# Kernel optimization log

Hardware: AMD Instinct MI355X
Metric: run time of the kernel (lower is better)

## Reference

```python
import jax, jax.numpy as jnp
import numpy as np

Q_DIM = 1024
K_DIM = 1024
HID = 128
EPS = 1e-5


def setup_inputs() -> dict:
    key = jax.random.key(0)
    ks = jax.random.split(key, 12)
    B, Tq, Tk = 2, 512, 512
    s_q = 1.0 / np.sqrt(Q_DIM)
    s_k = 1.0 / np.sqrt(K_DIM)
    s_h3 = 1.0 / np.sqrt(3 * HID)
    s_h = 1.0 / np.sqrt(HID)
    return {
        "Q": jax.random.normal(ks[0], (B, Tq, Q_DIM), jnp.float32),
        "K": jax.random.normal(ks[1], (B, Tk, K_DIM), jnp.float32),
        "Wq": jax.random.uniform(ks[2], (Q_DIM, HID), jnp.float32, -s_q, s_q),
        "Wk": jax.random.uniform(ks[3], (K_DIM, HID), jnp.float32, -s_k, s_k),
        "ln_g": jnp.ones((3 * HID,), jnp.float32),
        "ln_b": jnp.zeros((3 * HID,), jnp.float32),
        "Wu": jax.random.uniform(ks[4], (3 * HID, HID), jnp.float32, -s_h3, s_h3),
        "bu": jax.random.uniform(ks[5], (HID,), jnp.float32, -s_h3, s_h3),
        "Wv": jax.random.uniform(ks[6], (3 * HID, HID), jnp.float32, -s_h3, s_h3),
        "bv": jax.random.uniform(ks[7], (HID,), jnp.float32, -s_h3, s_h3),
        "Wo": jax.random.uniform(ks[8], (HID, 1), jnp.float32, -s_h, s_h),
        "bo": jax.random.uniform(ks[9], (1,), jnp.float32, -s_h, s_h),
    }


def reference(Q, K, Wq, Wk, ln_g, ln_b, Wu, bu, Wv, bv, Wo, bo):
    B, Tq, _ = Q.shape
    Tk = K.shape[1]
    q = jnp.einsum("bqd,dh->bqh", Q, Wq)              # (B,Tq,H)
    k = jnp.einsum("bkd,dh->bkh", K, Wk)              # (B,Tk,H)
    q_exp = jnp.broadcast_to(q[:, :, None, :], (B, Tq, Tk, HID))
    k_exp = jnp.broadcast_to(k[:, None, :, :], (B, Tq, Tk, HID))
    x = jnp.concatenate([q_exp, k_exp, q_exp * k_exp], axis=-1)  # (B,Tq,Tk,3H)
    mu = jnp.mean(x, axis=-1, keepdims=True)
    var = jnp.mean(jnp.square(x - mu), axis=-1, keepdims=True)
    x = (x - mu) * jax.lax.rsqrt(var + EPS) * ln_g + ln_b
    u = jnp.einsum("bqkc,ch->bqkh", x, Wu) + bu
    v = jnp.einsum("bqkc,ch->bqkh", x, Wv) + bv
    z = u * jax.nn.gelu(v, approximate=False)
    return (jnp.einsum("bqkh,ho->bqko", z, Wo) + bo)[..., 0]  # (B,Tq,Tk)
```

## Files before the change

### kernel.cpp

```cpp
#include <hip/hip_runtime.h>
#include <hip/hip_bf16.h>
#include <math.h>


#define EPSLN 1e-5f

#define WS_QP   0
#define WS_KP   131072
#define WS_PU   262144
#define WS_PV   393216
#define WS_RU   524288
#define WS_RV   655360
#define WS_SQ   786432
#define WS_QQ   787456
#define WS_SK   788480
#define WS_KK   789504
#define WS_GUS  790528
#define WS_GVS  790656
#define WS_CU   790784
#define WS_CV   790912
#define WS_WTU  791040
#define WS_WTV  815616
#define WS_WQT  840192
#define WS_WKT  905728

typedef __attribute__((ext_vector_type(8))) short short8;
typedef __attribute__((ext_vector_type(4))) float f32x4;

__device__ inline unsigned short f2bf(float x) {
    unsigned u = __builtin_bit_cast(unsigned, x);
    unsigned r = u + 0x7fffu + ((u >> 16) & 1u);
    return (unsigned short)(r >> 16);
}
__device__ inline float b2f_lo(unsigned v) { return __builtin_bit_cast(float, v << 16); }
__device__ inline float b2f_hi(unsigned v) { return __builtin_bit_cast(float, v & 0xffff0000u); }
__device__ inline unsigned pack_bf2(float a, float b) {
    __hip_bfloat162 h = __float22bfloat162_rn(make_float2(a, b));
    unsigned r;
    __builtin_memcpy(&r, &h, 4);
    return r;
}
__device__ inline void store8(unsigned short* p, const unsigned short* v) {
    short8 s;
    #pragma unroll
    for (int e = 0; e < 8; ++e) s[e] = (short)v[e];
    *(short8*)p = s;
}
#define GELU_C1 2.3022035f
#define GELU_C2 0.1029431f
__device__ inline float fast_gelu(float v) {
    float ex = __builtin_amdgcn_exp2f(v * fmaf(v * v, GELU_C2, GELU_C1));
    float r  = __builtin_amdgcn_rcpf(ex + 1.f);
    return v - v * r;
}
#define BAR_LDS() asm volatile("s_waitcnt lgkmcnt(0)\n\ts_barrier" ::: "memory")

__global__ __launch_bounds__(256, 2)
void k_prep(const float* __restrict__ Wu, const float* __restrict__ bu,
            const float* __restrict__ Wv, const float* __restrict__ bv,
            const float* __restrict__ g, const float* __restrict__ bln,
            const float* __restrict__ Wo,
            const float* __restrict__ Wq, const float* __restrict__ Wk,
            float* __restrict__ ws) {
    int task = blockIdx.x, t = threadIdx.x;
    if (task < 2) {
        bool isV = task != 0;
        const float* W  = isV ? Wv : Wu;
        const float* bb = isV ? bv : bu;
        float* gout = ws + (isV ? WS_GVS : WS_GUS);
        float* cout = ws + (isV ? WS_CV : WS_CU);
        __shared__ float rg[2][128], rc[2][128];
        int tl = t & 127, g2 = t >> 7;
        float gu = 0.f, cu = 0.f;
        #pragma unroll 4
        for (int c = g2 * 192; c < g2 * 192 + 192; ++c) {
            float wv_ = W[c * 128 + tl];
            gu += g[c] * wv_;
            cu += bln[c] * wv_;
        }
        rg[g2][tl] = gu; rc[g2][tl] = cu;
        __syncthreads();
        if (t < 128) gout[t] = rg[0][t] + rg[1][t];
        else { int h = t - 128; cout[h] = rc[0][h] + rc[1][h] + bb[h]; }
    } else if (task < 8) {
        int tt = task - 2;
        bool isV = tt >= 3;
        int seg = tt % 3;
        const float* W = isV ? Wv : Wu;
        unsigned short* wt = (unsigned short*)(ws + (isV ? WS_WTV : WS_WTU));
        __shared__ unsigned short tile[128 * 130];
        for (int it = 0; it < 64; ++it) {
            int idx = t + 256 * it;
            int c = idx >> 7, h = idx & 127;
            float s = g[seg * 128 + c] * (isV ? 1.f : Wo[h]);
            tile[c * 130 + h] = f2bf(s * W[(seg * 128 + c) * 128 + h]);
        }
        __syncthreads();
        int h = t >> 1, c0 = (t & 1) * 64;
        for (int cc = 0; cc < 64; cc += 8) {
            unsigned short v[8];
            #pragma unroll
            for (int e = 0; e < 8; ++e) v[e] = tile[(c0 + cc + e) * 130 + h];
            store8(&wt[h * 384 + seg * 128 + c0 + cc], v);
        }
    } else {
        int tt = task - 8;
        const float* W = (tt >> 3) ? Wk : Wq;
        unsigned short* wt = (unsigned short*)(ws + ((tt >> 3) ? WS_WKT : WS_WQT));
        int seg = tt & 7;
        __shared__ unsigned short tile[128 * 130];
        for (int it = 0; it < 64; ++it) {
            int idx = t + 256 * it;
            int c = idx >> 7, h = idx & 127;
            tile[c * 130 + h] = f2bf(W[(size_t)(seg * 128 + c) * 128 + h]);
        }
        __syncthreads();
        int h = t >> 1, c0 = (t & 1) * 64;
        for (int cc = 0; cc < 64; cc += 8) {
            unsigned short v[8];
            #pragma unroll
            for (int e = 0; e < 8; ++e) v[e] = tile[(c0 + cc + e) * 130 + h];
            store8(&wt[h * 1024 + seg * 128 + c0 + cc], v);
        }
    }
}

#define XST 1028
#define QST 132
__global__ __launch_bounds__(256, 2)
void k_proj(const float* __restrict__ Q, const float* __restrict__ K,
            float* __restrict__ ws) {
    int blk = blockIdx.x, t = threadIdx.x;
    bool isK = blk >= 128;
    int r0 = (blk & 127) * 8;
    const float* src = isK ? K : Q;
    const unsigned short* wtin = (const unsigned short*)(ws + (isK ? WS_WKT : WS_WQT));
    float* dst = ws + (isK ? WS_KP : WS_QP);
    int L = t & 63, w = t >> 6;
    int col = L & 15, quad = L >> 4;

    __shared__ unsigned short XLb[16 * XST];
    __shared__ unsigned short qpL[16 * QST];
    __shared__ float sp1[16][4], sp2[16][4];

    {
        int srow = t >> 5;
        int c0 = (t & 31) * 4;
        const float* sp = src + (size_t)(r0 + srow) * 1024;
        #pragma unroll
        for (int g8 = 0; g8 < 8; ++g8) {
            float4 xv = *(const float4*)(sp + g8 * 128 + c0);
            unsigned* xp = (unsigned*)&XLb[srow * XST + g8 * 128 + c0];
            xp[0] = pack_bf2(xv.x, xv.y);
            xp[1] = pack_bf2(xv.z, xv.w);
        }
    }
    __syncthreads();

    f32x4 acc[2];
    acc[0] = (f32x4){0.f, 0.f, 0.f, 0.f};
    acc[1] = (f32x4){0.f, 0.f, 0.f, 0.f};
    #pragma unroll 4
    for (int ks = 0; ks < 32; ++ks) {
        short8 a = *(const short8*)&XLb[col * XST + ks * 32 + quad * 8];
        #pragma unroll
        for (int nt2 = 0; nt2 < 2; ++nt2) {
            int h = w * 32 + nt2 * 16 + col;
            short8 b = *(const short8*)&wtin[(size_t)h * 1024 + ks * 32 + quad * 8];
            acc[nt2] = __builtin_amdgcn_mfma_f32_16x16x32_bf16(a, b, acc[nt2], 0, 0, 0);
        }
    }

    #pragma unroll
    for (int r = 0; r < 4; ++r) {
        int row = quad * 4 + r;
        float s1 = acc[0][r] + acc[1][r];
        float s2 = acc[0][r] * acc[0][r] + acc[1][r] * acc[1][r];
        #pragma unroll
        for (int d = 1; d < 16; d <<= 1) { s1 += __shfl_xor(s1, d); s2 += __shfl_xor(s2, d); }
        if (col == 0) { sp1[row][w] = s1; sp2[row][w] = s2; }
        #pragma unroll
        for (int nt2 = 0; nt2 < 2; ++nt2) {
            int h = w * 32 + nt2 * 16 + col;
            qpL[row * QST + h] = f2bf(acc[nt2][r]);
            if (row < 8) dst[(size_t)(r0 + row) * 128 + h] = acc[nt2][r];
        }
    }
    __syncthreads();
    if (t < 8) {
        ws[(isK ? WS_SK : WS_SQ) + r0 + t] = (sp1[t][0] + sp1[t][1]) + (sp1[t][2] + sp1[t][3]);
        ws[(isK ? WS_KK : WS_QQ) + r0 + t] = (sp2[t][0] + sp2[t][1]) + (sp2[t][2] + sp2[t][3]);
    }

    int uv = w & 1, nhf = w >> 1;
    const unsigned short* wt = (const unsigned short*)(ws + (uv ? WS_WTV : WS_WTU));
    int cb0 = isK ? 128 : 0;
    f32x4 pacc[4];
    #pragma unroll
    for (int nt = 0; nt < 4; ++nt) pacc[nt] = (f32x4){0.f, 0.f, 0.f, 0.f};
    #pragma unroll
    for (int ks = 0; ks < 4; ++ks) {
        short8 a = *(const short8*)&qpL[col * QST + ks * 32 + quad * 8];
        #pragma unroll
        for (int nt = 0; nt < 4; ++nt) {
            int h = nhf * 64 + nt * 16 + col;
            short8 b = *(const short8*)&wt[h * 384 + cb0 + ks * 32 + quad * 8];
            pacc[nt] = __builtin_amdgcn_mfma_f32_16x16x32_bf16(a, b, pacc[nt], 0, 0, 0);
        }
    }
    float* PO = ws + (uv ? (isK ? WS_RV : WS_PV) : (isK ? WS_RU : WS_PU));
    #pragma unroll
    for (int nt = 0; nt < 4; ++nt)
        #pragma unroll
        for (int r = 0; r < 4; ++r) {
            int row = quad * 4 + r;
            if (row < 8)
                PO[(size_t)(r0 + row) * 128 + nhf * 64 + nt * 16 + col] = pacc[nt][r];
        }
}

#define ASTR 152
#define REDS 132
#define PST  136
__global__ __launch_bounds__(1024, 4)
void k_main(const float* __restrict__ ws, float* __restrict__ out,
            const float* __restrict__ Wo, const float* __restrict__ bo) {
    int blk = blockIdx.x;
    int jt = blk & 7, ig = (blk >> 3) & 31, b = blk >> 8;
    int t = threadIdx.x;
    int L = t & 63, w = t >> 6;
    int col = L & 15, quad = L >> 4;
    int jh = w >> 3, wh = w & 7;
    int krow0 = b * 512 + jt * 64;
    int jj = t >> 4, cb = (t & 15) * 8;
    int h = wh * 16 + col;

    __shared__ __align__(16) char smem[61440];
    unsigned short* Alds = (unsigned short*)smem;
    float*          red2 = (float*)(smem + 19456);
    unsigned short* QL   = (unsigned short*)smem;
    unsigned short* Q2L  = (unsigned short*)(smem + 4352);
    unsigned short* KL   = (unsigned short*)(smem + 8704);
    unsigned short* K2L  = (unsigned short*)(smem + 26112);
    float*          rsL2 = (float*)(smem + 53248);

    int bi0 = b * 512 + ig * 16;

    float kreg[8];
    {
        const float* kp = ws + WS_KP + (size_t)(krow0 + jj) * 128 + cb;
        #pragma unroll
        for (int e = 0; e < 8; ++e) kreg[e] = kp[e];
        unsigned kk4[4], k2[4];
        #pragma unroll
        for (int e = 0; e < 4; ++e) {
            kk4[e] = pack_bf2(kreg[e * 2], kreg[e * 2 + 1]);
            k2[e]  = pack_bf2(kreg[e * 2] * kreg[e * 2], kreg[e * 2 + 1] * kreg[e * 2 + 1]);
        }
        *(uint4*)&KL[jj * PST + cb]  = *(uint4*)&kk4[0];
        *(uint4*)&K2L[jj * PST + cb] = *(uint4*)&k2[0];
    }
    if (t < 512) {
        int row = t >> 5, c0 = (t & 31) * 4;
        float4 qv = *(const float4*)(ws + WS_QP + (size_t)(bi0 + row) * 128 + c0);
        unsigned q01 = pack_bf2(qv.x, qv.y), q23 = pack_bf2(qv.z, qv.w);
        unsigned s01 = pack_bf2(qv.x * qv.x, qv.y * qv.y);
        unsigned s23 = pack_bf2(qv.z * qv.z, qv.w * qv.w);
        uint2 qp = make_uint2(q01, q23), sp = make_uint2(s01, s23);
        *(uint2*)&QL[row * PST + c0]  = qp;
        *(uint2*)&Q2L[row * PST + c0] = sp;
    }
    unsigned prR[8];
    #pragma unroll
    for (int mt = 0; mt < 2; ++mt)
        #pragma unroll
        for (int r = 0; r < 4; ++r) {
            int jl = jh * 32 + mt * 16 + quad * 4 + r;
            float ru = ws[WS_RU + (size_t)(krow0 + jl) * 128 + h];
            float rv = ws[WS_RV + (size_t)(krow0 + jl) * 128 + h];
            prR[mt * 4 + r] = pack_bf2(ru, rv);
        }

    short8 w3f[2][4];
    {
        const unsigned short* wtu = (const unsigned short*)(ws + WS_WTU);
        const unsigned short* wtv = (const unsigned short*)(ws + WS_WTV);
        #pragma unroll
        for (int ks = 0; ks < 4; ++ks) {
            w3f[0][ks] = *(const short8*)&wtu[h * 384 + 256 + ks * 32 + quad * 8];
            w3f[1][ks] = *(const short8*)&wtv[h * 384 + 256 + ks * 32 + quad * 8];
        }
    }
    float wo  = Wo[h];
    float gusv = ws[WS_GUS + h] * wo;
    float cuv  = ws[WS_CU + h] * wo;
    float gvsv = ws[WS_GVS + h];
    float cvv  = ws[WS_CV + h];
    float bo0 = bo[0];

    const float* qpBase = ws + WS_QP + (size_t)bi0 * 128 + cb;
    const float* puBase = ws + WS_PU + (size_t)bi0 * 128 + h;
    const float* pvBase = ws + WS_PV + (size_t)bi0 * 128 + h;
    float4 qA = *(const float4*)(qpBase);
    float4 qB = *(const float4*)(qpBase + 4);
    float puv = puBase[0];
    float pvv = pvBase[0];
    __syncthreads();

    if (w < 4) {
        int j = w * 16 + col;
        f32x4 d1a = (f32x4){0.f, 0.f, 0.f, 0.f};
        f32x4 d2a = (f32x4){0.f, 0.f, 0.f, 0.f};
        #pragma unroll
        for (int ks = 0; ks < 4; ++ks) {
            short8 aq  = *(const short8*)&QL[col * PST + ks * 32 + quad * 8];
            short8 bk  = *(const short8*)&KL[j * PST + ks * 32 + quad * 8];
            d1a = __builtin_amdgcn_mfma_f32_16x16x32_bf16(aq, bk, d1a, 0, 0, 0);
            short8 aq2 = *(const short8*)&Q2L[col * PST + ks * 32 + quad * 8];
            short8 bk2 = *(const short8*)&K2L[j * PST + ks * 32 + quad * 8];
            d2a = __builtin_amdgcn_mfma_f32_16x16x32_bf16(aq2, bk2, d2a, 0, 0, 0);
        }
        float skj = ws[WS_SK + krow0 + j];
        float kkj = ws[WS_KK + krow0 + j];
        #pragma unroll
        for (int r = 0; r < 4; ++r) {
            int i = quad * 4 + r;
            float mu = (ws[WS_SQ + bi0 + i] + skj + d1a[r]) * (1.0f / 384.0f);
            float e2 = (ws[WS_QQ + bi0 + i] + kkj + d2a[r]) * (1.0f / 384.0f);
            float rs = rsqrtf(e2 - mu * mu + EPSLN);
            *(float2*)&rsL2[(i * 64 + j) * 2] = make_float2(rs, rs * mu);
        }
    }
    __syncthreads();

    #pragma unroll 2
    for (int ii = 0; ii < 16; ++ii) {
        float4 qA2 = *(const float4*)(qpBase + (ii + 1) * 128);
        float4 qB2 = *(const float4*)(qpBase + (ii + 1) * 128 + 4);
        float pu2 = puBase[(ii + 1) * 128];
        float pv2 = pvBase[(ii + 1) * 128];
        {
            unsigned pk[4];
            float x0 = kreg[0] * qA.x, x1 = kreg[1] * qA.y;
            float x2 = kreg[2] * qA.z, x3 = kreg[3] * qA.w;
            float y0 = kreg[4] * qB.x, y1 = kreg[5] * qB.y;
            float y2 = kreg[6] * qB.z, y3 = kreg[7] * qB.w;
            pk[0] = pack_bf2(x0, x1); pk[1] = pack_bf2(x2, x3);
            pk[2] = pack_bf2(y0, y1); pk[3] = pack_bf2(y2, y3);
            unsigned* arow = (unsigned*)Alds + jj * (ASTR / 2) + cb / 2;
            *(uint4*)&arow[0] = *(uint4*)&pk[0];
        }
        BAR_LDS();
        f32x4 acc[2][2];
        #pragma unroll
        for (int mt = 0; mt < 2; ++mt) {
            acc[mt][0] = (f32x4){puv, puv, puv, puv};
            acc[mt][1] = (f32x4){pvv, pvv, pvv, pvv};
        }
        #pragma unroll
        for (int ks = 0; ks < 4; ++ks) {
            short8 a0 = *(const short8*)&Alds[(jh * 32 + col) * ASTR + ks * 32 + quad * 8];
            short8 a1 = *(const short8*)&Alds[(jh * 32 + col + 16) * ASTR + ks * 32 + quad * 8];
            acc[0][0] = __builtin_amdgcn_mfma_f32_16x16x32_bf16(a0, w3f[0][ks], acc[0][0], 0, 0, 0);
            acc[0][1] = __builtin_amdgcn_mfma_f32_16x16x32_bf16(a0, w3f[1][ks], acc[0][1], 0, 0, 0);
            acc[1][0] = __builtin_amdgcn_mfma_f32_16x16x32_bf16(a1, w3f[0][ks], acc[1][0], 0, 0, 0);
            acc[1][1] = __builtin_amdgcn_mfma_f32_16x16x32_bf16(a1, w3f[1][ks], acc[1][1], 0, 0, 0);
        }
        #pragma unroll
        for (int mt = 0; mt < 2; ++mt) {
            int jb = jh * 32 + mt * 16 + quad * 4;
            float4 s0 = *(const float4*)&rsL2[(ii * 64 + jb) * 2];
            float4 s1 = *(const float4*)&rsL2[(ii * 64 + jb) * 2 + 4];
            #pragma unroll
            for (int r = 0; r < 4; ++r) {
                float rs   = r == 0 ? s0.x : r == 1 ? s0.z : r == 2 ? s1.x : s1.z;
                float rsmu = r == 0 ? s0.y : r == 1 ? s0.w : r == 2 ? s1.y : s1.w;
                int jl = jb + r;
                unsigned pr = prR[mt * 4 + r];
                float su  = acc[mt][0][r] + b2f_lo(pr);
                float u   = fmaf(rs, su, fmaf(-rsmu, gusv, cuv));
                float sv_ = acc[mt][1][r] + b2f_hi(pr);
                float v   = fmaf(rs, sv_, fmaf(-rsmu, gvsv, cvv));
                red2[jl * REDS + wh * 16 + col] = u * fast_gelu(v);
            }
        }
        BAR_LDS();
        if (t < 512) {
            const float4* rr = (const float4*)&red2[(t >> 3) * REDS];
            int k = t & 7;
            float s = 0.f;
            #pragma unroll
            for (int c4 = 0; c4 < 4; ++c4) {
                float4 x = rr[k + c4 * 8];
                s += (x.x + x.y) + (x.z + x.w);
            }
            s += __shfl_xor(s, 1);
            s += __shfl_xor(s, 2);
            s += __shfl_xor(s, 4);
            if (k == 0)
                out[(size_t)(bi0 + ii) * 512 + jt * 64 + (t >> 3)] = s + bo0;
        }
        qA = qA2; qB = qB2; puv = pu2; pvv = pv2;
    }
}

extern "C" void kernel_launch(void* const* d_in, const int* in_sizes, int n_in,
                              void* d_out, int out_size, void* d_ws, size_t ws_size,
                              hipStream_t stream) {
    const float* Q   = (const float*)d_in[0];
    const float* K   = (const float*)d_in[1];
    const float* Wq  = (const float*)d_in[2];
    const float* Wk  = (const float*)d_in[3];
    const float* g   = (const float*)d_in[4];
    const float* bln = (const float*)d_in[5];
    const float* Wu  = (const float*)d_in[6];
    const float* bu  = (const float*)d_in[7];
    const float* Wv  = (const float*)d_in[8];
    const float* bv  = (const float*)d_in[9];
    const float* Wo  = (const float*)d_in[10];
    const float* bo  = (const float*)d_in[11];
    float* ws  = (float*)d_ws;
    float* out = (float*)d_out;

    hipLaunchKernelGGL(k_prep, dim3(24), dim3(256), 0, stream, Wu, bu, Wv, bv, g, bln, Wo, Wq, Wk, ws);
    hipLaunchKernelGGL(k_proj, dim3(256), dim3(256), 0, stream, Q, K, ws);
    hipLaunchKernelGGL(k_main, dim3(512), dim3(1024), 0, stream, ws, out, Wo, bo);
}
```

Baseline: 187.4 us.

## Halve k_main block tile and double-buffer LDS to drop one barrier per row

Each k_main block now covers 32 key columns with 512 threads instead of 64 with 1024, and the grid doubles to 1024 blocks. The A tile and the reduction buffer are double-buffered, and the row reduction for step ii-1 is deferred into step ii. That removes the second LDS barrier per iteration and lets the reduction overlap the next MFMA stage, with a final epilogue reduction after the loop. The cost is more blocks that each repeat setup work (loading K, Q, weights and the rs table) and more LDS per block.

```diff
diff --git a/kernel.cpp b/kernel.cpp
--- a/kernel.cpp
+++ b/kernel.cpp
@@ -222,27 +222,28 @@
 #define ASTR 152
 #define REDS 132
 #define PST  136
-__global__ __launch_bounds__(1024, 4)
+__global__ __launch_bounds__(512, 4)
 void k_main(const float* __restrict__ ws, float* __restrict__ out,
             const float* __restrict__ Wo, const float* __restrict__ bo) {
     int blk = blockIdx.x;
-    int jt = blk & 7, ig = (blk >> 3) & 31, b = blk >> 8;
+    int jt = blk & 15, ig = (blk >> 4) & 31, b = blk >> 9;
     int t = threadIdx.x;
     int L = t & 63, w = t >> 6;
     int col = L & 15, quad = L >> 4;
-    int jh = w >> 3, wh = w & 7;
-    int krow0 = b * 512 + jt * 64;
+    int krow0 = b * 512 + jt * 32;
     int jj = t >> 4, cb = (t & 15) * 8;
-    int h = wh * 16 + col;
-
-    __shared__ __align__(16) char smem[61440];
-    unsigned short* Alds = (unsigned short*)smem;
-    float*          red2 = (float*)(smem + 19456);
-    unsigned short* QL   = (unsigned short*)smem;
-    unsigned short* Q2L  = (unsigned short*)(smem + 4352);
-    unsigned short* KL   = (unsigned short*)(smem + 8704);
-    unsigned short* K2L  = (unsigned short*)(smem + 26112);
-    float*          rsL2 = (float*)(smem + 53248);
+    int h = w * 16 + col;
+
+    __shared__ __align__(16) char smem[57344];
+    unsigned short* Alds0 = (unsigned short*)smem;
+    unsigned short* Alds1 = (unsigned short*)(smem + 9728);
+    float*          red20 = (float*)(smem + 19456);
+    float*          red21 = (float*)(smem + 36352);
+    unsigned short* QL    = (unsigned short*)smem;
+    unsigned short* Q2L   = (unsigned short*)(smem + 4352);
+    unsigned short* KL    = (unsigned short*)(smem + 8704);
+    unsigned short* K2L   = (unsigned short*)(smem + 17408);
+    float*          rsL2  = (float*)(smem + 53248);
 
     int bi0 = b * 512 + ig * 16;
 
@@ -260,7 +261,7 @@
         *(uint4*)&KL[jj * PST + cb]  = *(uint4*)&kk4[0];
         *(uint4*)&K2L[jj * PST + cb] = *(uint4*)&k2[0];
     }
-    if (t < 512) {
+    {
         int row = t >> 5, c0 = (t & 31) * 4;
         float4 qv = *(const float4*)(ws + WS_QP + (size_t)(bi0 + row) * 128 + c0);
         unsigned q01 = pack_bf2(qv.x, qv.y), q23 = pack_bf2(qv.z, qv.w);
@@ -275,7 +276,7 @@
     for (int mt = 0; mt < 2; ++mt)
         #pragma unroll
         for (int r = 0; r < 4; ++r) {
-            int jl = jh * 32 + mt * 16 + quad * 4 + r;
+            int jl = mt * 16 + quad * 4 + r;
             float ru = ws[WS_RU + (size_t)(krow0 + jl) * 128 + h];
             float rv = ws[WS_RV + (size_t)(krow0 + jl) * 128 + h];
             prR[mt * 4 + r] = pack_bf2(ru, rv);
@@ -307,7 +308,7 @@
     float pvv = pvBase[0];
     __syncthreads();
 
-    if (w < 4) {
+    if (w < 2) {
         int j = w * 16 + col;
         f32x4 d1a = (f32x4){0.f, 0.f, 0.f, 0.f};
         f32x4 d2a = (f32x4){0.f, 0.f, 0.f, 0.f};
@@ -328,13 +329,16 @@
             float mu = (ws[WS_SQ + bi0 + i] + skj + d1a[r]) * (1.0f / 384.0f);
             float e2 = (ws[WS_QQ + bi0 + i] + kkj + d2a[r]) * (1.0f / 384.0f);
             float rs = rsqrtf(e2 - mu * mu + EPSLN);
-            *(float2*)&rsL2[(i * 64 + j) * 2] = make_float2(rs, rs * mu);
+            *(float2*)&rsL2[(i * 32 + j) * 2] = make_float2(rs, rs * mu);
         }
     }
     __syncthreads();
 
     #pragma unroll 2
     for (int ii = 0; ii < 16; ++ii) {
+        unsigned short* Ap = (ii & 1) ? Alds1 : Alds0;
+        float* Rp = (ii & 1) ? red21 : red20;
+        float* Rq = (ii & 1) ? red20 : red21;
         float4 qA2 = *(const float4*)(qpBase + (ii + 1) * 128);
         float4 qB2 = *(const float4*)(qpBase + (ii + 1) * 128 + 4);
         float pu2 = puBase[(ii + 1) * 128];
@@ -347,7 +351,7 @@
             float y2 = kreg[6] * qB.z, y3 = kreg[7] * qB.w;
             pk[0] = pack_bf2(x0, x1); pk[1] = pack_bf2(x2, x3);
             pk[2] = pack_bf2(y0, y1); pk[3] = pack_bf2(y2, y3);
-            unsigned* arow = (unsigned*)Alds + jj * (ASTR / 2) + cb / 2;
+            unsigned* arow = (unsigned*)Ap + jj * (ASTR / 2) + cb / 2;
             *(uint4*)&arow[0] = *(uint4*)&pk[0];
         }
         BAR_LDS();
@@ -359,34 +363,15 @@
         }
         #pragma unroll
         for (int ks = 0; ks < 4; ++ks) {
-            short8 a0 = *(const short8*)&Alds[(jh * 32 + col) * ASTR + ks * 32 + quad * 8];
-            short8 a1 = *(const short8*)&Alds[(jh * 32 + col + 16) * ASTR + ks * 32 + quad * 8];
+            short8 a0 = *(const short8*)&Ap[col * ASTR + ks * 32 + quad * 8];
+            short8 a1 = *(const short8*)&Ap[(col + 16) * ASTR + ks * 32 + quad * 8];
             acc[0][0] = __builtin_amdgcn_mfma_f32_16x16x32_bf16(a0, w3f[0][ks], acc[0][0], 0, 0, 0);
             acc[0][1] = __builtin_amdgcn_mfma_f32_16x16x32_bf16(a0, w3f[1][ks], acc[0][1], 0, 0, 0);
             acc[1][0] = __builtin_amdgcn_mfma_f32_16x16x32_bf16(a1, w3f[0][ks], acc[1][0], 0, 0, 0);
             acc[1][1] = __builtin_amdgcn_mfma_f32_16x16x32_bf16(a1, w3f[1][ks], acc[1][1], 0, 0, 0);
         }
-        #pragma unroll
-        for (int mt = 0; mt < 2; ++mt) {
-            int jb = jh * 32 + mt * 16 + quad * 4;
-            float4 s0 = *(const float4*)&rsL2[(ii * 64 + jb) * 2];
-            float4 s1 = *(const float4*)&rsL2[(ii * 64 + jb) * 2 + 4];
-            #pragma unroll
-            for (int r = 0; r < 4; ++r) {
-                float rs   = r == 0 ? s0.x : r == 1 ? s0.z : r == 2 ? s1.x : s1.z;
-                float rsmu = r == 0 ? s0.y : r == 1 ? s0.w : r == 2 ? s1.y : s1.w;
-                int jl = jb + r;
-                unsigned pr = prR[mt * 4 + r];
-                float su  = acc[mt][0][r] + b2f_lo(pr);
-                float u   = fmaf(rs, su, fmaf(-rsmu, gusv, cuv));
-                float sv_ = acc[mt][1][r] + b2f_hi(pr);
-                float v   = fmaf(rs, sv_, fmaf(-rsmu, gvsv, cvv));
-                red2[jl * REDS + wh * 16 + col] = u * fast_gelu(v);
-            }
-        }
-        BAR_LDS();
-        if (t < 512) {
-            const float4* rr = (const float4*)&red2[(t >> 3) * REDS];
+        if (ii > 0 && t < 256) {
+            const float4* rr = (const float4*)&Rq[(t >> 3) * REDS];
             int k = t & 7;
             float s = 0.f;
             #pragma unroll
@@ -398,9 +383,43 @@
             s += __shfl_xor(s, 2);
             s += __shfl_xor(s, 4);
             if (k == 0)
-                out[(size_t)(bi0 + ii) * 512 + jt * 64 + (t >> 3)] = s + bo0;
+                out[(size_t)(bi0 + ii - 1) * 512 + jt * 32 + (t >> 3)] = s + bo0;
+        }
+        #pragma unroll
+        for (int mt = 0; mt < 2; ++mt) {
+            int jb = mt * 16 + quad * 4;
+            float4 s0 = *(const float4*)&rsL2[(ii * 32 + jb) * 2];
+            float4 s1 = *(const float4*)&rsL2[(ii * 32 + jb) * 2 + 4];
+            #pragma unroll
+            for (int r = 0; r < 4; ++r) {
+                float rs   = r == 0 ? s0.x : r == 1 ? s0.z : r == 2 ? s1.x : s1.z;
+                float rsmu = r == 0 ? s0.y : r == 1 ? s0.w : r == 2 ? s1.y : s1.w;
+                int jl = jb + r;
+                unsigned pr = prR[mt * 4 + r];
+                float su  = acc[mt][0][r] + b2f_lo(pr);
+                float u   = fmaf(rs, su, fmaf(-rsmu, gusv, cuv));
+                float sv_ = acc[mt][1][r] + b2f_hi(pr);
+                float v   = fmaf(rs, sv_, fmaf(-rsmu, gvsv, cvv));
+                Rp[jl * REDS + w * 16 + col] = u * fast_gelu(v);
+            }
         }
         qA = qA2; qB = qB2; puv = pu2; pvv = pv2;
+    }
+    BAR_LDS();
+    if (t < 256) {
+        const float4* rr = (const float4*)&red21[(t >> 3) * REDS];
+        int k = t & 7;
+        float s = 0.f;
+        #pragma unroll
+        for (int c4 = 0; c4 < 4; ++c4) {
+            float4 x = rr[k + c4 * 8];
+            s += (x.x + x.y) + (x.z + x.w);
+        }
+        s += __shfl_xor(s, 1);
+        s += __shfl_xor(s, 2);
+        s += __shfl_xor(s, 4);
+        if (k == 0)
+            out[(size_t)(bi0 + 15) * 512 + jt * 32 + (t >> 3)] = s + bo0;
     }
 }
 
@@ -424,5 +443,5 @@
 
     hipLaunchKernelGGL(k_prep, dim3(24), dim3(256), 0, stream, Wu, bu, Wv, bv, g, bln, Wo, Wq, Wk, ws);
     hipLaunchKernelGGL(k_proj, dim3(256), dim3(256), 0, stream, Q, K, ws);
-    hipLaunchKernelGGL(k_main, dim3(512), dim3(1024), 0, stream, ws, out, Wo, bo);
-}
+    hipLaunchKernelGGL(k_main, dim3(1024), dim3(512), 0, stream, ws, out, Wo, bo);
+}
```

New measurement: 174.3 us. -7.0%, faster.
